# Kernel optimization log

Hardware: AMD Instinct MI355X
Metric: run time of the kernel (lower is better)

Reference implementation:

```python
import jax, jax.numpy as jnp
import numpy as np

FEAT_H = 32
FEAT_W = 32
GAUSS_THR = 0.6
GAUSS_3D_THR = 0.5
GAUSS_DEPTH_THR = 0.5
EXPAND = 1.2     # roi_expand_param
SIGMA = 1.6
BIN_OFFSET = 0.5
B, N, M = 4, 1024, 64


def setup_inputs() -> dict:
    key = jax.random.key(0)
    k1, k2, k3, k4, k5, k6, k7, k8, k9 = jax.random.split(key, 9)
    # ground-truth boxes inside a ~1024x768 image
    gx1 = jax.random.uniform(k1, (B, M)) * 800.0
    gy1 = jax.random.uniform(k2, (B, M)) * 600.0
    gw = jax.random.uniform(k3, (B, M)) * 200.0 + 32.0
    gh = jax.random.uniform(k4, (B, M)) * 200.0 + 32.0
    gt_box = jnp.stack([gx1, gy1, gx1 + gw, gy1 + gh], axis=-1)          # (B,M,4)
    # keypoint = (approx) box center, label in {0,1,2} (0 = ignore)
    kx = gx1 + 0.5 * gw + jax.random.normal(k5, (B, M)) * 2.0
    ky = gy1 + 0.5 * gh + jax.random.normal(k5, (B, M)) * 2.0
    klabel = jax.random.randint(k6, (B, M), 0, 3).astype(jnp.float32)
    dims = jax.random.uniform(k7, (B, M, 3)) * 3.0 + 0.5                 # l,h,w
    loc = jnp.concatenate([
        jax.random.normal(k8, (B, M, 2)) * 10.0,
        jax.random.uniform(k8, (B, M, 1)) * 75.0 + 5.0], axis=-1)       # x,y,depth
    rot = (jax.random.uniform(k9, (B, M, 1)) * 2.0 - 1.0) * np.pi
    gt_boxes = jnp.concatenate(
        [gt_box, kx[..., None], ky[..., None], klabel[..., None], dims, loc, rot],
        axis=-1).astype(jnp.float32)                                     # (B,M,14)
    match_gt_id = jax.random.randint(k2, (B, N), 0, M)
    matched4 = jnp.take_along_axis(gt_box, match_gt_id[..., None], axis=1)
    boxes = (matched4 + jax.random.normal(k3, (B, N, 4)) * 8.0).astype(jnp.float32)
    match_pos_flag = jax.random.randint(k4, (B, N), 0, 2).astype(jnp.int32)
    return {"boxes": boxes, "gt_boxes": gt_boxes,
            "match_pos_flag": match_pos_flag, "match_gt_id": match_gt_id}


def _forward(boxes, gt_boxes, match_pos_flag, match_gt_id):
    H, W = FEAT_H, FEAT_W
    dt = boxes.dtype
    # take_row: matched gt per proposal
    matched = jnp.take_along_axis(gt_boxes, match_gt_id[..., None], axis=1)  # (B,N,14)
    x1, y1, x2, y2 = (boxes[..., i] for i in range(4))
    # zoom_boxes: expand about center by roi_expand_param
    cx, cy = 0.5 * (x1 + x2), 0.5 * (y1 + y2)
    hw, hh = 0.5 * (x2 - x1) * EXPAND, 0.5 * (y2 - y1) * EXPAND
    ex1, ey1, ex2, ey2 = cx - hw, cy - hh, cx + hw, cy + hh
    sx = W / (ex2 - ex1 + 1.0)
    sy = H / (ey2 - ey1 + 1.0)
    kx = (matched[..., 4] - ex1) * sx                                    # (B,N)
    ky = (matched[..., 5] - ey1) * sy
    vis = matched[..., 6] != 0                                           # ignore_labels=(0,)
    valid = vis & (match_pos_flag > 0)                                   # (B,N)
    gx = jnp.arange(W, dtype=dt)[None, None, None, :]                    # bin x (cols)
    gy = jnp.arange(H, dtype=dt)[None, None, :, None]                    # bin y (rows)
    kxe, kye = kx[..., None, None], ky[..., None, None]
    two_sig2 = 2.0 * SIGMA * SIGMA
    score = jnp.exp(-(((gx + BIN_OFFSET - kxe) ** 2 +
                       (gy + BIN_OFFSET - kye) ** 2) / two_sig2))        # (B,N,H,W)
    offx = kxe - gx                                                      # (B,N,1,W), radius=1
    offy = kye - gy                                                      # (B,N,H,1)
    vmask = valid[..., None, None]
    m2 = (score >= GAUSS_THR) & vmask
    has = jnp.any(m2, axis=(-2, -1))                                     # (B,N) len(keep_pos)>0
    hasf = has[..., None, None].astype(dt)
    cls_label = jnp.where(has[..., None, None], score, -1.0)[:, :, None]           # (B,N,1,H,W)
    cls_label_w = jnp.broadcast_to(hasf, score.shape)[:, :, None]
    m2f = m2.astype(dt)
    reg_2d = jnp.stack([jnp.broadcast_to(offx * m2f, score.shape),
                        jnp.broadcast_to(offy * m2f, score.shape)], axis=2)         # (B,N,2,H,W)
    reg_2d_w = jnp.stack([m2f, m2f], axis=2)
    m3f = ((score >= GAUSS_3D_THR) & vmask).astype(dt)
    reg_3d = jnp.stack([jnp.broadcast_to(offx * m3f, score.shape),
                        jnp.broadcast_to(offy * m3f, score.shape)], axis=2)
    reg_3d_w = jnp.stack([m3f, m3f], axis=2)
    mdf = ((score >= GAUSS_DEPTH_THR) & vmask).astype(dt)
    depth = matched[..., 12][..., None, None]
    depth_label = (depth * mdf)[:, :, None]
    depth_label_w = mdf[:, :, None]
    dims = matched[..., 7:10]                                            # (B,N,3)
    dim_label = dims[..., None, None] * m3f[:, :, None]                  # (B,N,3,H,W)
    dim_label_w = jnp.broadcast_to(m3f[:, :, None], dim_label.shape)
    rot = matched[..., 13][..., None, None]
    rot_label = (rot * m3f)[:, :, None]
    rot_label_w = m3f[:, :, None]
    return (cls_label, cls_label_w, reg_2d, reg_2d_w, reg_3d, reg_3d_w,
            depth_label, depth_label_w, dim_label, dim_label_w,
            rot_label, rot_label_w)


def reference(boxes, gt_boxes, match_pos_flag, match_gt_id):
    return _forward(boxes, gt_boxes, match_pos_flag, match_gt_id)
```

## Files before the change

kernel.cpp:

```cpp
#include <hip/hip_runtime.h>

constexpr int B = 4, N = 1024, M = 64, H = 32, W = 32;
constexpr float EXPAND = 1.2f;
constexpr float TWO_SIG2 = 2.0f * 1.6f * 1.6f;
constexpr float GAUSS_THR = 0.6f;
constexpr float GAUSS_3D_THR = 0.5f;
constexpr int HW = H * W;
constexpr size_t S = (size_t)B * N * HW;

typedef float vfloat4 __attribute__((ext_vector_type(4)));


__global__ __launch_bounds__(256)
void rcnn3d_label_kernel(const float* __restrict__ boxes,
                         const float* __restrict__ gt_boxes,
                         const int*   __restrict__ pos_flag,
                         const int*   __restrict__ gt_id,
                         float* __restrict__ out)
{
    const int bn  = blockIdx.x;
    const int b   = bn >> 10;
    const int tid = threadIdx.x;

    const float4 bx = *reinterpret_cast<const float4*>(boxes + (size_t)bn * 4);
    const int   gid = gt_id[bn];
    const float* g  = gt_boxes + ((size_t)b * M + gid) * 14;
    const float kxg = g[4], kyg = g[5], klab = g[6];
    const float dim0 = g[7], dim1 = g[8], dim2 = g[9];
    const float depth = g[12], rot = g[13];
    const bool valid = (klab != 0.0f) && (pos_flag[bn] > 0);

    const float cx = 0.5f * (bx.x + bx.z);
    const float cy = 0.5f * (bx.y + bx.w);
    const float hw = 0.5f * (bx.z - bx.x) * EXPAND;
    const float hh = 0.5f * (bx.w - bx.y) * EXPAND;
    const float ex1 = cx - hw, ey1 = cy - hh;
    const float ex2 = cx + hw, ey2 = cy + hh;
    const float sx = (float)W / (ex2 - ex1 + 1.0f);
    const float sy = (float)H / (ey2 - ey1 + 1.0f);
    const float kx = (kxg - ex1) * sx;
    const float ky = (kyg - ey1) * sy;

    const float nxf = fminf(fmaxf(floorf(kx), 0.0f), 31.0f);
    const float nyf = fminf(fmaxf(floorf(ky), 0.0f), 31.0f);
    const float dxn = nxf + 0.5f - kx;
    const float dyn = nyf + 0.5f - ky;
    const float dyn2 = dyn * dyn;
    const float smax = expf(-((dxn * dxn + dyn2) / TWO_SIG2));
    const bool  has  = valid && (smax >= GAUSS_THR);

    const int h  = tid >> 3;
    const int w0 = (tid & 7) * 4;
    const float gy   = (float)h;
    const float offy = ky - gy;
    const float dy   = gy + 0.5f - ky;
    const float dy2  = dy * dy;

    float score[4], offx[4];
    bool  m2[4], m3[4];
#pragma unroll
    for (int j = 0; j < 4; ++j) {
        const float gx = (float)(w0 + j);
        const float dx = gx + 0.5f - kx;
        const float s  = expf(-((dx * dx + dy2) / TWO_SIG2));
        score[j] = s;
        offx[j]  = kx - gx;
        m2[j] = (s >= GAUSS_THR)    && valid;
        m3[j] = (s >= GAUSS_3D_THR) && valid;
    }

    vfloat4 v_cls, v_clsw, v_rx2, v_ry2, v_w2, v_rx3, v_ry3, v_w3;
    vfloat4 v_dep, v_d0, v_d1, v_d2, v_rot;
#pragma unroll
    for (int j = 0; j < 4; ++j) {
        const float f2 = m2[j] ? 1.0f : 0.0f;
        const float f3 = m3[j] ? 1.0f : 0.0f;
        v_cls[j]  = has ? score[j] : -1.0f;
        v_clsw[j] = has ? 1.0f : 0.0f;
        v_rx2[j]  = offx[j] * f2;
        v_ry2[j]  = offy    * f2;
        v_w2[j]   = f2;
        v_rx3[j]  = offx[j] * f3;
        v_ry3[j]  = offy    * f3;
        v_w3[j]   = f3;
        v_dep[j]  = depth * f3;
        v_d0[j]   = dim0 * f3;
        v_d1[j]   = dim1 * f3;
        v_d2[j]   = dim2 * f3;
        v_rot[j]  = rot * f3;
    }

    const size_t cell = (size_t)tid * 4;
    const size_t bn1  = (size_t)bn * HW;
    const size_t bn2  = (size_t)bn * 2 * HW;
    const size_t bn3  = (size_t)bn * 3 * HW;
    auto st = [&](size_t ofs, const vfloat4& v) {
        __builtin_nontemporal_store(v, reinterpret_cast<vfloat4*>(out + ofs + cell));
    };

    st( 0 * S + bn1,            v_cls);
    st( 1 * S + bn1,            v_clsw);
    st( 2 * S + bn2,            v_rx2);
    st( 2 * S + bn2 + HW,       v_ry2);
    st( 4 * S + bn2,            v_w2);
    st( 4 * S + bn2 + HW,       v_w2);
    st( 6 * S + bn2,            v_rx3);
    st( 6 * S + bn2 + HW,       v_ry3);
    st( 8 * S + bn2,            v_w3);
    st( 8 * S + bn2 + HW,       v_w3);
    st(10 * S + bn1,            v_dep);
    st(11 * S + bn1,            v_w3);
    st(12 * S + bn3,            v_d0);
    st(12 * S + bn3 + HW,       v_d1);
    st(12 * S + bn3 + 2 * HW,   v_d2);
    st(15 * S + bn3,            v_w3);
    st(15 * S + bn3 + HW,       v_w3);
    st(15 * S + bn3 + 2 * HW,   v_w3);
    st(18 * S + bn1,            v_rot);
    st(19 * S + bn1,            v_w3);
}

extern "C" void kernel_launch(void* const* d_in, const int* in_sizes, int n_in,
                              void* d_out, int out_size, void* d_ws, size_t ws_size,
                              hipStream_t stream) {
    const float* boxes    = (const float*)d_in[0];
    const float* gt_boxes = (const float*)d_in[1];
    const int*   pos_flag = (const int*)d_in[2];
    const int*   gt_id    = (const int*)d_in[3];
    float*       out      = (float*)d_out;

    rcnn3d_label_kernel<<<dim3(B * N), dim3(256), 0, stream>>>(
        boxes, gt_boxes, pos_flag, gt_id, out);
}
```

Measured before the change: 334.7 us.

## Split work per output channel so each block streams one contiguous channel

Blocks now each handle one output channel for a chunk of 32 proposals, rather than one proposal across all 20 channels. The goal is contiguous write streams per block, avoiding the scattered writes to 20 distant regions. Per-proposal setup is computed once per block into shared memory. The cost is that the gaussian and the setup are recomputed once per channel, and channel metadata is looked up from constant tables.

```diff
diff --git a/kernel.cpp b/kernel.cpp
--- a/kernel.cpp
+++ b/kernel.cpp
@@ -7,9 +7,68 @@
 constexpr float GAUSS_3D_THR = 0.5f;
 constexpr int HW = H * W;
 constexpr size_t S = (size_t)B * N * HW;
+constexpr int BN = B * N;
+constexpr int CHUNK = 32;
+constexpr int NCHUNK = BN / CHUNK;
+constexpr int NCC = 20;
 
 typedef float vfloat4 __attribute__((ext_vector_type(4)));
 
+
+enum Kind { K_CLS, K_CLSW, K_RX2, K_RY2, K_W2, K_RX3, K_RY3, K_W3, K_AUX3 };
+
+__constant__ int d_kind[NCC] = {K_CLS, K_CLSW, K_RX2, K_RY2, K_W2, K_W2,
+                                K_RX3, K_RY3, K_W3, K_W3, K_AUX3, K_W3,
+                                K_AUX3, K_AUX3, K_AUX3, K_W3, K_W3, K_W3,
+                                K_AUX3, K_W3};
+__constant__ int d_base[NCC] = {0, 1, 2, 2, 4, 4, 6, 6, 8, 8,
+                                10, 11, 12, 12, 12, 15, 15, 15, 18, 19};
+__constant__ int d_hwof[NCC] = {0, 0, 0, 1, 0, 1, 0, 1, 0, 1,
+                                0, 0, 0, 1, 2, 0, 1, 2, 0, 0};
+__constant__ int d_nch[NCC]  = {1, 1, 2, 2, 2, 2, 2, 2, 2, 2,
+                                1, 1, 3, 3, 3, 3, 3, 3, 1, 1};
+__constant__ int d_aux[NCC]  = {7, 7, 7, 7, 7, 7, 7, 7, 7, 7,
+                                12, 7, 7, 8, 9, 7, 7, 7, 13, 7};
+
+template <int KIND>
+__device__ __forceinline__ void run_loop(int bn0, int nch, int w0, float gy,
+                                         const float* p_kx, const float* p_ky,
+                                         const float* p_val, const float* p_has,
+                                         const float* p_aux, float* outc)
+{
+#pragma unroll 8
+    for (int i = 0; i < CHUNK; ++i) {
+        const int bn   = bn0 + i;
+        const float kx = p_kx[i], ky = p_ky[i];
+        const float vf = p_val[i], hf = p_has[i], ax = p_aux[i];
+        const float dy   = gy + 0.5f - ky;
+        const float dy2  = dy * dy;
+        const float offy = ky - gy;
+        vfloat4 v;
+#pragma unroll
+        for (int j = 0; j < 4; ++j) {
+            const float gx = (float)(w0 + j);
+            float r;
+            if constexpr (KIND == K_CLSW) {
+                r = hf;
+            } else {
+                const float dx = gx + 0.5f - kx;
+                const float s  = expf(-((dx * dx + dy2) / TWO_SIG2));
+                if constexpr (KIND == K_CLS)  r = (hf != 0.0f) ? s : -1.0f;
+                if constexpr (KIND == K_RX2)  r = (kx - gx) * ((s >= GAUSS_THR)    ? vf : 0.0f);
+                if constexpr (KIND == K_RY2)  r = offy      * ((s >= GAUSS_THR)    ? vf : 0.0f);
+                if constexpr (KIND == K_W2)   r =             ((s >= GAUSS_THR)    ? vf : 0.0f);
+                if constexpr (KIND == K_RX3)  r = (kx - gx) * ((s >= GAUSS_3D_THR) ? vf : 0.0f);
+                if constexpr (KIND == K_RY3)  r = offy      * ((s >= GAUSS_3D_THR) ? vf : 0.0f);
+                if constexpr (KIND == K_W3)   r =             ((s >= GAUSS_3D_THR) ? vf : 0.0f);
+                if constexpr (KIND == K_AUX3) r = ax        * ((s >= GAUSS_3D_THR) ? vf : 0.0f);
+            }
+            v[j] = r;
+        }
+        __builtin_nontemporal_store(
+            v, reinterpret_cast<vfloat4*>(outc + (size_t)bn * nch * HW));
+    }
+}
 
 __global__ __launch_bounds__(256)
 void rcnn3d_label_kernel(const float* __restrict__ boxes,
@@ -18,106 +77,69 @@
                          const int*   __restrict__ gt_id,
                          float* __restrict__ out)
 {
-    const int bn  = blockIdx.x;
-    const int b   = bn >> 10;
-    const int tid = threadIdx.x;
+    const int bid   = blockIdx.x;
+    const int cc    = bid / NCHUNK;
+    const int chunk = bid % NCHUNK;
+    const int bn0   = chunk * CHUNK;
+    const int tid   = threadIdx.x;
 
-    const float4 bx = *reinterpret_cast<const float4*>(boxes + (size_t)bn * 4);
-    const int   gid = gt_id[bn];
-    const float* g  = gt_boxes + ((size_t)b * M + gid) * 14;
-    const float kxg = g[4], kyg = g[5], klab = g[6];
-    const float dim0 = g[7], dim1 = g[8], dim2 = g[9];
-    const float depth = g[12], rot = g[13];
-    const bool valid = (klab != 0.0f) && (pos_flag[bn] > 0);
+    const int kind = d_kind[cc];
+    const int auxi = d_aux[cc];
+    const int nch  = d_nch[cc];
+    const size_t cbase = (size_t)d_base[cc] * S + (size_t)d_hwof[cc] * HW;
 
-    const float cx = 0.5f * (bx.x + bx.z);
-    const float cy = 0.5f * (bx.y + bx.w);
-    const float hw = 0.5f * (bx.z - bx.x) * EXPAND;
-    const float hh = 0.5f * (bx.w - bx.y) * EXPAND;
-    const float ex1 = cx - hw, ey1 = cy - hh;
-    const float ex2 = cx + hw, ey2 = cy + hh;
-    const float sx = (float)W / (ex2 - ex1 + 1.0f);
-    const float sy = (float)H / (ey2 - ey1 + 1.0f);
-    const float kx = (kxg - ex1) * sx;
-    const float ky = (kyg - ey1) * sy;
+    __shared__ float p_kx[CHUNK], p_ky[CHUNK], p_val[CHUNK], p_has[CHUNK], p_aux[CHUNK];
+    if (tid < CHUNK) {
+        const int bn = bn0 + tid;
+        const int b  = bn >> 10;
+        const float4 bx = *reinterpret_cast<const float4*>(boxes + (size_t)bn * 4);
+        const int   gi  = gt_id[bn];
+        const float* g  = gt_boxes + ((size_t)b * M + gi) * 14;
 
-    const float nxf = fminf(fmaxf(floorf(kx), 0.0f), 31.0f);
-    const float nyf = fminf(fmaxf(floorf(ky), 0.0f), 31.0f);
-    const float dxn = nxf + 0.5f - kx;
-    const float dyn = nyf + 0.5f - ky;
-    const float dyn2 = dyn * dyn;
-    const float smax = expf(-((dxn * dxn + dyn2) / TWO_SIG2));
-    const bool  has  = valid && (smax >= GAUSS_THR);
+        const float cx = 0.5f * (bx.x + bx.z);
+        const float cy = 0.5f * (bx.y + bx.w);
+        const float hw = 0.5f * (bx.z - bx.x) * EXPAND;
+        const float hh = 0.5f * (bx.w - bx.y) * EXPAND;
+        const float ex1 = cx - hw, ey1 = cy - hh;
+        const float ex2 = cx + hw, ey2 = cy + hh;
+        const float sx = (float)W / (ex2 - ex1 + 1.0f);
+        const float sy = (float)H / (ey2 - ey1 + 1.0f);
+        const float kx = (g[4] - ex1) * sx;
+        const float ky = (g[5] - ey1) * sy;
+        const bool valid = (g[6] != 0.0f) && (pos_flag[bn] > 0);
+
+        const float nxf = fminf(fmaxf(floorf(kx), 0.0f), 31.0f);
+        const float nyf = fminf(fmaxf(floorf(ky), 0.0f), 31.0f);
+        const float dxn = nxf + 0.5f - kx;
+        const float dyn = nyf + 0.5f - ky;
+        const float dyn2 = dyn * dyn;
+        const float smax = expf(-((dxn * dxn + dyn2) / TWO_SIG2));
+        const bool  has  = valid && (smax >= GAUSS_THR);
+
+        p_kx[tid]  = kx;
+        p_ky[tid]  = ky;
+        p_val[tid] = valid ? 1.0f : 0.0f;
+        p_has[tid] = has ? 1.0f : 0.0f;
+        p_aux[tid] = g[auxi];
+    }
+    __syncthreads();
 
     const int h  = tid >> 3;
     const int w0 = (tid & 7) * 4;
-    const float gy   = (float)h;
-    const float offy = ky - gy;
-    const float dy   = gy + 0.5f - ky;
-    const float dy2  = dy * dy;
+    const float gy = (float)h;
+    float* outc = out + cbase + (size_t)tid * 4;
 
-    float score[4], offx[4];
-    bool  m2[4], m3[4];
-#pragma unroll
-    for (int j = 0; j < 4; ++j) {
-        const float gx = (float)(w0 + j);
-        const float dx = gx + 0.5f - kx;
-        const float s  = expf(-((dx * dx + dy2) / TWO_SIG2));
-        score[j] = s;
-        offx[j]  = kx - gx;
-        m2[j] = (s >= GAUSS_THR)    && valid;
-        m3[j] = (s >= GAUSS_3D_THR) && valid;
+    switch (kind) {
+        case K_CLS:  run_loop<K_CLS >(bn0, nch, w0, gy, p_kx, p_ky, p_val, p_has, p_aux, outc); break;
+        case K_CLSW: run_loop<K_CLSW>(bn0, nch, w0, gy, p_kx, p_ky, p_val, p_has, p_aux, outc); break;
+        case K_RX2:  run_loop<K_RX2 >(bn0, nch, w0, gy, p_kx, p_ky, p_val, p_has, p_aux, outc); break;
+        case K_RY2:  run_loop<K_RY2 >(bn0, nch, w0, gy, p_kx, p_ky, p_val, p_has, p_aux, outc); break;
+        case K_W2:   run_loop<K_W2  >(bn0, nch, w0, gy, p_kx, p_ky, p_val, p_has, p_aux, outc); break;
+        case K_RX3:  run_loop<K_RX3 >(bn0, nch, w0, gy, p_kx, p_ky, p_val, p_has, p_aux, outc); break;
+        case K_RY3:  run_loop<K_RY3 >(bn0, nch, w0, gy, p_kx, p_ky, p_val, p_has, p_aux, outc); break;
+        case K_W3:   run_loop<K_W3  >(bn0, nch, w0, gy, p_kx, p_ky, p_val, p_has, p_aux, outc); break;
+        default:     run_loop<K_AUX3>(bn0, nch, w0, gy, p_kx, p_ky, p_val, p_has, p_aux, outc); break;
     }
-
-    vfloat4 v_cls, v_clsw, v_rx2, v_ry2, v_w2, v_rx3, v_ry3, v_w3;
-    vfloat4 v_dep, v_d0, v_d1, v_d2, v_rot;
-#pragma unroll
-    for (int j = 0; j < 4; ++j) {
-        const float f2 = m2[j] ? 1.0f : 0.0f;
-        const float f3 = m3[j] ? 1.0f : 0.0f;
-        v_cls[j]  = has ? score[j] : -1.0f;
-        v_clsw[j] = has ? 1.0f : 0.0f;
-        v_rx2[j]  = offx[j] * f2;
-        v_ry2[j]  = offy    * f2;
-        v_w2[j]   = f2;
-        v_rx3[j]  = offx[j] * f3;
-        v_ry3[j]  = offy    * f3;
-        v_w3[j]   = f3;
-        v_dep[j]  = depth * f3;
-        v_d0[j]   = dim0 * f3;
-        v_d1[j]   = dim1 * f3;
-        v_d2[j]   = dim2 * f3;
-        v_rot[j]  = rot * f3;
-    }
-
-    const size_t cell = (size_t)tid * 4;
-    const size_t bn1  = (size_t)bn * HW;
-    const size_t bn2  = (size_t)bn * 2 * HW;
-    const size_t bn3  = (size_t)bn * 3 * HW;
-    auto st = [&](size_t ofs, const vfloat4& v) {
-        __builtin_nontemporal_store(v, reinterpret_cast<vfloat4*>(out + ofs + cell));
-    };
-
-    st( 0 * S + bn1,            v_cls);
-    st( 1 * S + bn1,            v_clsw);
-    st( 2 * S + bn2,            v_rx2);
-    st( 2 * S + bn2 + HW,       v_ry2);
-    st( 4 * S + bn2,            v_w2);
-    st( 4 * S + bn2 + HW,       v_w2);
-    st( 6 * S + bn2,            v_rx3);
-    st( 6 * S + bn2 + HW,       v_ry3);
-    st( 8 * S + bn2,            v_w3);
-    st( 8 * S + bn2 + HW,       v_w3);
-    st(10 * S + bn1,            v_dep);
-    st(11 * S + bn1,            v_w3);
-    st(12 * S + bn3,            v_d0);
-    st(12 * S + bn3 + HW,       v_d1);
-    st(12 * S + bn3 + 2 * HW,   v_d2);
-    st(15 * S + bn3,            v_w3);
-    st(15 * S + bn3 + HW,       v_w3);
-    st(15 * S + bn3 + 2 * HW,   v_w3);
-    st(18 * S + bn1,            v_rot);
-    st(19 * S + bn1,            v_w3);
 }
 
 extern "C" void kernel_launch(void* const* d_in, const int* in_sizes, int n_in,
@@ -129,6 +151,6 @@
     const int*   gt_id    = (const int*)d_in[3];
     float*       out      = (float*)d_out;
 
-    rcnn3d_label_kernel<<<dim3(B * N), dim3(256), 0, stream>>>(
+    rcnn3d_label_kernel<<<dim3(NCC * NCHUNK), dim3(256), 0, stream>>>(
         boxes, gt_boxes, pos_flag, gt_id, out);
 }
```

New measurement: 342.0 us. +2.2%, slower.
